# Kernel optimization log

Hardware: AMD Instinct MI355X
Metric: run time of the kernel (lower is better)

Reference implementation:

```python
import jax, jax.numpy as jnp
import numpy as np

NUM_HEADS = 8
HIDDEN = 128
MAX_NEIGHBORS = 64
BATCH = 8192


def setup_inputs() -> dict:
    key = jax.random.key(0)
    ks = jax.random.split(key, 4)
    query = jax.random.normal(ks[0], (BATCH, MAX_NEIGHBORS, HIDDEN), dtype=jnp.float32)
    value = jax.random.normal(ks[1], (BATCH, 1, HIDDEN), dtype=jnp.float32)
    # per-head Dense(hidden) weights (glorot-ish scale) + zero biases
    Wa = jax.random.normal(ks[2], (NUM_HEADS, HIDDEN, HIDDEN), dtype=jnp.float32) * (1.0 / np.sqrt(HIDDEN))
    ba = jnp.zeros((NUM_HEADS, HIDDEN), dtype=jnp.float32)
    Wo = jax.random.normal(ks[3], (NUM_HEADS * HIDDEN, HIDDEN), dtype=jnp.float32) * (1.0 / np.sqrt(NUM_HEADS * HIDDEN))
    bo = jnp.zeros((HIDDEN,), dtype=jnp.float32)
    return {"query": query, "value": value, "Wa": Wa, "ba": ba, "Wo": Wo, "bo": bo}


def reference(query, value, Wa, ba, Wo, bo):
    # query: [B, N, H], value: [B, 1, H]
    q = jnp.concatenate([query, value], axis=1)  # [B, N+1, H]
    contexts = []
    for i in range(NUM_HEADS):
        # sequential per-head projection of the running query tensor
        q = jnp.einsum('bnh,hk->bnk', q, Wa[i]) + ba[i]          # [B, N+1, H]
        e = jnp.einsum('boh,bnh->bon', value, q)                 # [B, 1, N+1]
        scores = jax.nn.softmax(e, axis=-1)                      # [B, 1, N+1]
        contexts.append(jnp.einsum('bon,bnh->boh', scores, q))   # [B, 1, H]
    ctx = jnp.concatenate(contexts, axis=-1)                     # [B, 1, num_heads*H]
    x = jnp.einsum('boc,ck->bok', ctx, Wo) + bo                  # [B, 1, H]
    return jax.nn.relu(x)
```

## Files before the change

kernel.cpp:

```cpp
#include <hip/hip_runtime.h>
#include <math.h>

#define WS_P  0
#define WS_Q0 65536
#define WS_Q1 81920
#define WS_R  98304
#define WS_WT 114688
#define WS_WU 245760
#define WS_ZT 376832
#define WS_Z0 507904
#define WS_U  524288
#define WS_PO 8912896

struct MMJob { const float* A; const float* B; float* C; float* wu; };
struct MMArgs { MMJob j[8]; };

__device__ __forceinline__ float dpp_xor1(float x) {
  return __int_as_float(__builtin_amdgcn_update_dpp(0, __float_as_int(x), 0xB1, 0xF, 0xF, false));
}
__device__ __forceinline__ float dpp_xor2(float x) {
  return __int_as_float(__builtin_amdgcn_update_dpp(0, __float_as_int(x), 0x4E, 0xF, 0xF, false));
}
__device__ __forceinline__ float dpp_xor8(float x) {
  return __int_as_float(__builtin_amdgcn_update_dpp(0, __float_as_int(x), 0x128, 0xF, 0xF, false));
}
__device__ __forceinline__ float readlane_f(float v, int n) {
  return __int_as_float(__builtin_amdgcn_readlane(__float_as_int(v), n));
}

__device__ void mm128_job(const MMJob J, const int tile, const int t, float* Al) {
  const int col = t & 127;
  const int rg = t >> 7;
  if (J.A == nullptr) {
    for (int rr = 0; rr < 16; ++rr) {
      const int r = tile * 32 + rg * 16 + rr;
      const float v = J.B[r * 128 + col];
      if (J.C) J.C[r * 128 + col] = v;
      if (J.wu) J.wu[col * 1024 + r] = v;
    }
    return;
  }
  for (int jj = 0; jj < 16; ++jj) {
    const int idx = t + jj * 256;
    Al[idx] = J.A[tile * 32 * 128 + idx];
  }
  __syncthreads();
  float acc[16];
#pragma unroll
  for (int rr = 0; rr < 16; ++rr) acc[rr] = 0.f;
  for (int h = 0; h < 128; ++h) {
    const float bv = J.B[h * 128 + col];
#pragma unroll
    for (int rr = 0; rr < 16; ++rr)
      acc[rr] = fmaf(Al[(rg * 16 + rr) * 128 + h], bv, acc[rr]);
  }
#pragma unroll
  for (int rr = 0; rr < 16; ++rr) {
    const int r = tile * 32 + rg * 16 + rr;
    if (J.C) J.C[r * 128 + col] = acc[rr];
    if (J.wu) J.wu[col * 1024 + r] = acc[rr];
  }
}

__global__ __launch_bounds__(256) void mm128_jobs(MMArgs args) {
  __shared__ float smem[4096];
  mm128_job(args.j[blockIdx.x >> 2], blockIdx.x & 3, threadIdx.x, smem);
}

__device__ void bias_z0_dev(const float* __restrict__ Wa, const float* __restrict__ ba,
                            const float* __restrict__ Wo, const float* __restrict__ bo,
                            float* __restrict__ z0, const int t, float* smem) {
  float* bt = smem;
  float* zpart = smem + 1024;
  if (t < 128) bt[t] = ba[t];
  __syncthreads();
  for (int i = 1; i < 8; ++i) {
    if (t < 128) {
      float v = ba[i * 128 + t];
      for (int h = 0; h < 128; ++h)
        v = fmaf(bt[(i - 1) * 128 + h], Wa[i * 16384 + h * 128 + t], v);
      bt[i * 128 + t] = v;
    }
    __syncthreads();
  }
  const int col = t & 127, half = t >> 7;
  float z = half ? 0.f : bo[col];
  for (int i = half * 4; i < half * 4 + 4; ++i)
    for (int h = 0; h < 128; ++h)
      z = fmaf(bt[i * 128 + h], Wo[(i * 128 + h) * 128 + col], z);
  zpart[half * 128 + col] = z;
  __syncthreads();
  if (t < 128) z0[t] = zpart[t] + zpart[128 + t];
}

__device__ void gemm_U_dev(const float* __restrict__ V, const float* __restrict__ WU,
                           float* __restrict__ U, const int bid, const int t, float* Vl) {
  const int rt = bid >> 3;
  const int ct = bid & 7;
  const int cg = t & 7;
  const int rg = t >> 3;
  const int r0 = rt * 128;
  float4 acc[4][4];
#pragma unroll
  for (int a = 0; a < 4; ++a)
#pragma unroll
    for (int c = 0; c < 4; ++c) acc[a][c] = make_float4(0.f, 0.f, 0.f, 0.f);
  for (int kc = 0; kc < 4; ++kc) {
    __syncthreads();
    {
      const int srow = t >> 3, k8 = t & 7;
#pragma unroll
      for (int pp = 0; pp < 4; ++pp) {
        const int rr = pp * 32 + srow;
        *(float4*)&Vl[rr * 33 + k8 * 4] =
            *(const float4*)&V[(size_t)(r0 + rr) * 128 + kc * 32 + k8 * 4];
      }
    }
    __syncthreads();
#pragma unroll 4
    for (int kk = 0; kk < 32; ++kk) {
      const float* wrow = WU + (size_t)(kc * 32 + kk) * 1024 + ct * 128 + cg * 16;
      const float4 w0 = *(const float4*)(wrow + 0);
      const float4 w1 = *(const float4*)(wrow + 4);
      const float4 w2 = *(const float4*)(wrow + 8);
      const float4 w3 = *(const float4*)(wrow + 12);
#pragma unroll
      for (int r = 0; r < 4; ++r) {
        const float s = Vl[(rg * 4 + r) * 33 + kk];
        acc[r][0].x = fmaf(s, w0.x, acc[r][0].x); acc[r][0].y = fmaf(s, w0.y, acc[r][0].y);
        acc[r][0].z = fmaf(s, w0.z, acc[r][0].z); acc[r][0].w = fmaf(s, w0.w, acc[r][0].w);
        acc[r][1].x = fmaf(s, w1.x, acc[r][1].x); acc[r][1].y = fmaf(s, w1.y, acc[r][1].y);
        acc[r][1].z = fmaf(s, w1.z, acc[r][1].z); acc[r][1].w = fmaf(s, w1.w, acc[r][1].w);
        acc[r][2].x = fmaf(s, w2.x, acc[r][2].x); acc[r][2].y = fmaf(s, w2.y, acc[r][2].y);
        acc[r][2].z = fmaf(s, w2.z, acc[r][2].z); acc[r][2].w = fmaf(s, w2.w, acc[r][2].w);
        acc[r][3].x = fmaf(s, w3.x, acc[r][3].x); acc[r][3].y = fmaf(s, w3.y, acc[r][3].y);
        acc[r][3].z = fmaf(s, w3.z, acc[r][3].z); acc[r][3].w = fmaf(s, w3.w, acc[r][3].w);
      }
    }
  }
#pragma unroll
  for (int r = 0; r < 4; ++r) {
    float* urow = U + (size_t)(r0 + rg * 4 + r) * 1024 + ct * 128 + cg * 16;
    *(float4*)(urow + 0) = acc[r][0];
    *(float4*)(urow + 4) = acc[r][1];
    *(float4*)(urow + 8) = acc[r][2];
    *(float4*)(urow + 12) = acc[r][3];
  }
}

__global__ __launch_bounds__(256) void k4_combo(MMArgs args,
    const float* __restrict__ V, const float* __restrict__ WU, float* __restrict__ U,
    const float* __restrict__ Wa, const float* __restrict__ ba,
    const float* __restrict__ Wo, const float* __restrict__ bo,
    float* __restrict__ z0) {
  __shared__ float smem[4224];
  const int bid = blockIdx.x;
  if (bid < 32) mm128_job(args.j[bid >> 2], bid & 3, threadIdx.x, smem);
  else if (bid < 544) gemm_U_dev(V, WU, U, bid - 32, threadIdx.x, smem);
  else bias_z0_dev(Wa, ba, Wo, bo, z0, threadIdx.x, smem);
}

__global__ __launch_bounds__(256, 4) void attn_main_k(
    const float* __restrict__ query, const float* __restrict__ value,
    float* __restrict__ U) {
  __shared__ float epart[8 * 66];
  __shared__ float spart[4 * 1024];
  const int b = blockIdx.x;
  const int t = threadIdx.x;
  const int w = t >> 6;
  const int l = t & 63;

  const int sel1 = l & 1, sel2 = (l >> 1) & 1, sel8 = (l >> 3) & 1;
  const int g = ((l >> 2) & 1) | (((l >> 4) & 1) << 1) | (((l >> 5) & 1) << 2);
  const int myhead = 4 * sel1 + 2 * sel2 + sel8;

  float2 u2[8];
  {
    const float* ub = U + (size_t)b * 1024 + 2 * l;
#pragma unroll
    for (int jj = 0; jj < 8; ++jj) u2[jj] = *(const float2*)(ub + ((myhead ^ jj) << 7));
  }
  float2 q2[16];
  {
    const float* qb = query + (size_t)b * 8192 + (size_t)(w * 16) * 128 + 2 * l;
#pragma unroll
    for (int r = 0; r < 16; ++r) q2[r] = *(const float2*)(qb + r * 128);
  }
  const float2 v2 = *(const float2*)(value + (size_t)b * 128 + 2 * l);

  auto epass = [&](const float2 qv, const int n) {
    float p[8];
#pragma unroll
    for (int i = 0; i < 8; ++i) p[i] = fmaf(qv.y, u2[i].y, qv.x * u2[i].x);
    float a4[4];
#pragma unroll
    for (int i = 0; i < 4; ++i) a4[i] = p[i] + dpp_xor1(p[i + 4]);
    float a2v[2];
#pragma unroll
    for (int i = 0; i < 2; ++i) a2v[i] = a4[i] + dpp_xor2(a4[i + 2]);
    float e = a2v[0] + dpp_xor8(a2v[1]);
    e += __shfl_xor(e, 4);
    e += __shfl_xor(e, 16);
    e += __shfl_xor(e, 32);
    if (g == 0) epart[myhead * 66 + n] = e;
  };
#pragma unroll
  for (int r = 0; r < 16; ++r) epass(q2[r], 16 * w + r);
  if (w == 0) epass(v2, 64);
  __syncthreads();

  float sc[8], c64[8];
  {
#pragma unroll
    for (int i = 0; i < 8; ++i) {
      const float x = epart[i * 66 + l];
      const float x64 = epart[i * 66 + 64];
      float m = x;
      m = fmaxf(m, dpp_xor1(m));
      m = fmaxf(m, dpp_xor2(m));
      m = fmaxf(m, __shfl_xor(m, 4));
      m = fmaxf(m, dpp_xor8(m));
      m = fmaxf(m, __shfl_xor(m, 16));
      m = fmaxf(m, __shfl_xor(m, 32));
      m = fmaxf(m, x64);
      const float p = __expf(x - m);
      const float p64 = __expf(x64 - m);
      float ss = p;
      ss += dpp_xor1(ss);
      ss += dpp_xor2(ss);
      ss += __shfl_xor(ss, 4);
      ss += dpp_xor8(ss);
      ss += __shfl_xor(ss, 16);
      ss += __shfl_xor(ss, 32);
      ss += p64;
      const float inv = 1.0f / ss;
      sc[i] = p * inv;
      c64[i] = p64 * inv;
    }
  }

  float2 s2[8];
#pragma unroll
  for (int i = 0; i < 8; ++i) s2[i] = make_float2(0.f, 0.f);
#pragma unroll
  for (int r = 0; r < 16; ++r) {
    const int n = 16 * w + r;
#pragma unroll
    for (int i = 0; i < 8; ++i) {
      const float cwv = readlane_f(sc[i], n);
      s2[i].x = fmaf(cwv, q2[r].x, s2[i].x);
      s2[i].y = fmaf(cwv, q2[r].y, s2[i].y);
    }
  }
  if (w == 0) {
#pragma unroll
    for (int i = 0; i < 8; ++i) {
      s2[i].x = fmaf(c64[i], v2.x, s2[i].x);
      s2[i].y = fmaf(c64[i], v2.y, s2[i].y);
    }
  }
#pragma unroll
  for (int i = 0; i < 8; ++i)
    *(float2*)&spart[w * 1024 + i * 128 + 2 * l] = s2[i];
  __syncthreads();
  float4 acc = make_float4(0.f, 0.f, 0.f, 0.f);
#pragma unroll
  for (int w4 = 0; w4 < 4; ++w4) {
    const float4 pp = *(const float4*)&spart[w4 * 1024 + t * 4];
    acc.x += pp.x; acc.y += pp.y; acc.z += pp.z; acc.w += pp.w;
  }
  *(float4*)(U + (size_t)b * 1024 + t * 4) = acc;
}

__global__ __launch_bounds__(256) void gemm_out_k(
    const float* __restrict__ S, const float* __restrict__ Z,
    float* __restrict__ P0, float* __restrict__ PW) {
  __shared__ float STl[64 * 68];
  const int rb = blockIdx.x >> 2;
  const int kc = blockIdx.x & 3;
  const int t = threadIdx.x;
  const int rg = t >> 4;
  const int cg = t & 15;
  float4 acc[4][2];
#pragma unroll
  for (int r = 0; r < 4; ++r) {
    acc[r][0] = make_float4(0.f, 0.f, 0.f, 0.f);
    acc[r][1] = make_float4(0.f, 0.f, 0.f, 0.f);
  }
  for (int sub = 0; sub < 4; ++sub) {
    const int kb = kc * 256 + sub * 64;
    __syncthreads();
#pragma unroll
    for (int j = 0; j < 4; ++j) {
      const int i4 = t + j * 256;
      const int row = i4 >> 4, kq = i4 & 15;
      const float4 s4 = *(const float4*)&S[(size_t)(rb * 64 + row) * 1024 + kb + kq * 4];
      STl[(kq * 4 + 0) * 68 + row] = s4.x;
      STl[(kq * 4 + 1) * 68 + row] = s4.y;
      STl[(kq * 4 + 2) * 68 + row] = s4.z;
      STl[(kq * 4 + 3) * 68 + row] = s4.w;
    }
    __syncthreads();
#pragma unroll 4
    for (int k = 0; k < 64; ++k) {
      const float4 sa = *(const float4*)&STl[k * 68 + rg * 4];
      const float* zr = Z + (size_t)(kb + k) * 128 + cg * 8;
      const float4 za = *(const float4*)zr;
      const float4 zb = *(const float4*)(zr + 4);
      const float sr[4] = {sa.x, sa.y, sa.z, sa.w};
#pragma unroll
      for (int r = 0; r < 4; ++r) {
        acc[r][0].x = fmaf(sr[r], za.x, acc[r][0].x);
        acc[r][0].y = fmaf(sr[r], za.y, acc[r][0].y);
        acc[r][0].z = fmaf(sr[r], za.z, acc[r][0].z);
        acc[r][0].w = fmaf(sr[r], za.w, acc[r][0].w);
        acc[r][1].x = fmaf(sr[r], zb.x, acc[r][1].x);
        acc[r][1].y = fmaf(sr[r], zb.y, acc[r][1].y);
        acc[r][1].z = fmaf(sr[r], zb.z, acc[r][1].z);
        acc[r][1].w = fmaf(sr[r], zb.w, acc[r][1].w);
      }
    }
  }
  float* P = (kc == 0) ? P0 : (PW + (size_t)(kc - 1) * 1048576);
#pragma unroll
  for (int r = 0; r < 4; ++r) {
    float* prow = P + (size_t)(rb * 64 + rg * 4 + r) * 128 + cg * 8;
    *(float4*)(prow + 0) = acc[r][0];
    *(float4*)(prow + 4) = acc[r][1];
  }
}

__global__ __launch_bounds__(256) void reduce_relu_k(
    float* __restrict__ out, const float* __restrict__ PW,
    const float* __restrict__ z0) {
  const int idx = blockIdx.x * 256 + threadIdx.x;
  const float4 z4 = *(const float4*)&z0[(idx & 31) * 4];
  float4 a = ((const float4*)out)[idx];
  const float4 p1 = ((const float4*)(PW + 0 * 1048576))[idx];
  const float4 p2 = ((const float4*)(PW + 1 * 1048576))[idx];
  const float4 p3 = ((const float4*)(PW + 2 * 1048576))[idx];
  a.x = fmaxf(a.x + p1.x + p2.x + p3.x + z4.x, 0.f);
  a.y = fmaxf(a.y + p1.y + p2.y + p3.y + z4.y, 0.f);
  a.z = fmaxf(a.z + p1.z + p2.z + p3.z + z4.z, 0.f);
  a.w = fmaxf(a.w + p1.w + p2.w + p3.w + z4.w, 0.f);
  ((float4*)out)[idx] = a;
}

extern "C" void kernel_launch(void* const* d_in, const int* in_sizes, int n_in,
                              void* d_out, int out_size, void* d_ws, size_t ws_size,
                              hipStream_t stream) {
  const float* query = (const float*)d_in[0];
  const float* value = (const float*)d_in[1];
  const float* Wa    = (const float*)d_in[2];
  const float* ba    = (const float*)d_in[3];
  const float* Wo    = (const float*)d_in[4];
  const float* bo    = (const float*)d_in[5];
  float* ws = (float*)d_ws;
  float* P  = ws + WS_P;
  float* Q0 = ws + WS_Q0;
  float* Q1 = ws + WS_Q1;
  float* R  = ws + WS_R;
  float* WT = ws + WS_WT;
  float* WU = ws + WS_WU;
  float* ZT = ws + WS_ZT;
  float* Z0 = ws + WS_Z0;
  float* U  = ws + WS_U;
  float* PW = ws + WS_PO;

  MMArgs a1{};
  for (int j = 0; j < 4; ++j)
    a1.j[j] = MMJob{Wa + 2 * j * 16384, Wa + (2 * j + 1) * 16384, P + j * 16384, nullptr};
  mm128_jobs<<<16, 256, 0, stream>>>(a1);

  MMArgs a2{};
  a2.j[0] = MMJob{P, P + 16384, Q0, nullptr};
  a2.j[1] = MMJob{P + 2 * 16384, P + 3 * 16384, Q1, nullptr};
  a2.j[2] = MMJob{P + 2 * 16384, Wa + 6 * 16384, R, nullptr};
  mm128_jobs<<<12, 256, 0, stream>>>(a2);

  MMArgs a3{};
  a3.j[0] = MMJob{nullptr, Wa,             WT + 0 * 16384, WU + 0 * 128};
  a3.j[1] = MMJob{nullptr, P,              WT + 1 * 16384, WU + 1 * 128};
  a3.j[2] = MMJob{P,       Wa + 2 * 16384, WT + 2 * 16384, WU + 2 * 128};
  a3.j[3] = MMJob{nullptr, Q0,             WT + 3 * 16384, WU + 3 * 128};
  a3.j[4] = MMJob{Q0,      Wa + 4 * 16384, WT + 4 * 16384, WU + 4 * 128};
  a3.j[5] = MMJob{Q0,      P + 2 * 16384,  WT + 5 * 16384, WU + 5 * 128};
  a3.j[6] = MMJob{Q0,      R,              WT + 6 * 16384, WU + 6 * 128};
  a3.j[7] = MMJob{Q0,      Q1,             WT + 7 * 16384, WU + 7 * 128};
  mm128_jobs<<<32, 256, 0, stream>>>(a3);

  MMArgs a4{};
  for (int i = 0; i < 8; ++i)
    a4.j[i] = MMJob{WT + i * 16384, Wo + i * 16384, ZT + i * 16384, nullptr};
  k4_combo<<<545, 256, 0, stream>>>(a4, value, WU, U, Wa, ba, Wo, bo, Z0);

  attn_main_k<<<8192, 256, 0, stream>>>(query, value, U);

  gemm_out_k<<<512, 256, 0, stream>>>(U, ZT, (float*)d_out, PW);
  reduce_relu_k<<<1024, 256, 0, stream>>>((float*)d_out, PW, Z0);
}
```

Baseline: 234.7 us.

## Assign one batch row per wavefront in attention kernel, removing block syncs

Restructures the attention kernel so each 64-lane wave processes a full batch row, streaming query in 16-row chunks instead of splitting rows across four waves. This removes the __syncthreads barriers and the shared-memory cross-wave partial-sum reduction, and cuts the grid to 2048 blocks. In exchange, the query row is loaded twice from global memory (once for scores, once for the weighted sum). This risks doubling HBM traffic on a memory-bound kernel if the re-read misses cache.

Result: slower. 261.2 us (+11.3%).

```diff
diff --git a/kernel.cpp b/kernel.cpp
--- a/kernel.cpp
+++ b/kernel.cpp
@@ -160,15 +160,15 @@
   else bias_z0_dev(Wa, ba, Wo, bo, z0, threadIdx.x, smem);
 }
 
-__global__ __launch_bounds__(256, 4) void attn_main_k(
+__global__ __launch_bounds__(256, 4) void attn_wave_k(
     const float* __restrict__ query, const float* __restrict__ value,
     float* __restrict__ U) {
-  __shared__ float epart[8 * 66];
-  __shared__ float spart[4 * 1024];
-  const int b = blockIdx.x;
+  __shared__ float etab[4 * 544];
   const int t = threadIdx.x;
   const int w = t >> 6;
   const int l = t & 63;
+  const int b = blockIdx.x * 4 + w;
+  float* et = etab + w * 544;
 
   const int sel1 = l & 1, sel2 = (l >> 1) & 1, sel8 = (l >> 3) & 1;
   const int g = ((l >> 2) & 1) | (((l >> 4) & 1) << 1) | (((l >> 5) & 1) << 2);
@@ -180,12 +180,7 @@
 #pragma unroll
     for (int jj = 0; jj < 8; ++jj) u2[jj] = *(const float2*)(ub + ((myhead ^ jj) << 7));
   }
-  float2 q2[16];
-  {
-    const float* qb = query + (size_t)b * 8192 + (size_t)(w * 16) * 128 + 2 * l;
-#pragma unroll
-    for (int r = 0; r < 16; ++r) q2[r] = *(const float2*)(qb + r * 128);
-  }
+  const float* qb = query + (size_t)b * 8192 + 2 * l;
   const float2 v2 = *(const float2*)(value + (size_t)b * 128 + 2 * l);
 
   auto epass = [&](const float2 qv, const int n) {
@@ -202,74 +197,77 @@
     e += __shfl_xor(e, 4);
     e += __shfl_xor(e, 16);
     e += __shfl_xor(e, 32);
-    if (g == 0) epart[myhead * 66 + n] = e;
+    if (g == 0) et[myhead * 66 + n] = e;
   };
-#pragma unroll
-  for (int r = 0; r < 16; ++r) epass(q2[r], 16 * w + r);
-  if (w == 0) epass(v2, 64);
-  __syncthreads();
+
+#pragma unroll 1
+  for (int c = 0; c < 4; ++c) {
+    float2 qc[16];
+#pragma unroll
+    for (int r = 0; r < 16; ++r) qc[r] = *(const float2*)(qb + (c * 16 + r) * 128);
+#pragma unroll
+    for (int r = 0; r < 16; ++r) epass(qc[r], c * 16 + r);
+  }
+  epass(v2, 64);
+  asm volatile("s_waitcnt lgkmcnt(0)" ::: "memory");
 
   float sc[8], c64[8];
+#pragma unroll
+  for (int i = 0; i < 8; ++i) {
+    const float x = et[i * 66 + l];
+    const float x64 = et[i * 66 + 64];
+    float m = x;
+    m = fmaxf(m, dpp_xor1(m));
+    m = fmaxf(m, dpp_xor2(m));
+    m = fmaxf(m, __shfl_xor(m, 4));
+    m = fmaxf(m, dpp_xor8(m));
+    m = fmaxf(m, __shfl_xor(m, 16));
+    m = fmaxf(m, __shfl_xor(m, 32));
+    m = fmaxf(m, x64);
+    const float p = __expf(x - m);
+    const float p64 = __expf(x64 - m);
+    float ss = p;
+    ss += dpp_xor1(ss);
+    ss += dpp_xor2(ss);
+    ss += __shfl_xor(ss, 4);
+    ss += dpp_xor8(ss);
+    ss += __shfl_xor(ss, 16);
+    ss += __shfl_xor(ss, 32);
+    ss += p64;
+    const float inv = 1.0f / ss;
+    sc[i] = p * inv;
+    c64[i] = p64 * inv;
+  }
+
+  float2 s2[8];
+#pragma unroll
+  for (int i = 0; i < 8; ++i) s2[i] = make_float2(0.f, 0.f);
+#pragma unroll 1
+  for (int c = 0; c < 4; ++c) {
+    float2 qc[16];
+#pragma unroll
+    for (int r = 0; r < 16; ++r) qc[r] = *(const float2*)(qb + (c * 16 + r) * 128);
+#pragma unroll
+    for (int r = 0; r < 16; ++r) {
+      const int n = c * 16 + r;
+#pragma unroll
+      for (int i = 0; i < 8; ++i) {
+        const float cwv = readlane_f(sc[i], n);
+        s2[i].x = fmaf(cwv, qc[r].x, s2[i].x);
+        s2[i].y = fmaf(cwv, qc[r].y, s2[i].y);
+      }
+    }
+  }
+#pragma unroll
+  for (int i = 0; i < 8; ++i) {
+    s2[i].x = fmaf(c64[i], v2.x, s2[i].x);
+    s2[i].y = fmaf(c64[i], v2.y, s2[i].y);
+  }
   {
-#pragma unroll
-    for (int i = 0; i < 8; ++i) {
-      const float x = epart[i * 66 + l];
-      const float x64 = epart[i * 66 + 64];
-      float m = x;
-      m = fmaxf(m, dpp_xor1(m));
-      m = fmaxf(m, dpp_xor2(m));
-      m = fmaxf(m, __shfl_xor(m, 4));
-      m = fmaxf(m, dpp_xor8(m));
-      m = fmaxf(m, __shfl_xor(m, 16));
-      m = fmaxf(m, __shfl_xor(m, 32));
-      m = fmaxf(m, x64);
-      const float p = __expf(x - m);
-      const float p64 = __expf(x64 - m);
-      float ss = p;
-      ss += dpp_xor1(ss);
-      ss += dpp_xor2(ss);
-      ss += __shfl_xor(ss, 4);
-      ss += dpp_xor8(ss);
-      ss += __shfl_xor(ss, 16);
-      ss += __shfl_xor(ss, 32);
-      ss += p64;
-      const float inv = 1.0f / ss;
-      sc[i] = p * inv;
-      c64[i] = p64 * inv;
-    }
-  }
-
-  float2 s2[8];
-#pragma unroll
-  for (int i = 0; i < 8; ++i) s2[i] = make_float2(0.f, 0.f);
-#pragma unroll
-  for (int r = 0; r < 16; ++r) {
-    const int n = 16 * w + r;
-#pragma unroll
-    for (int i = 0; i < 8; ++i) {
-      const float cwv = readlane_f(sc[i], n);
-      s2[i].x = fmaf(cwv, q2[r].x, s2[i].x);
-      s2[i].y = fmaf(cwv, q2[r].y, s2[i].y);
-    }
-  }
-  if (w == 0) {
-#pragma unroll
-    for (int i = 0; i < 8; ++i) {
-      s2[i].x = fmaf(c64[i], v2.x, s2[i].x);
-      s2[i].y = fmaf(c64[i], v2.y, s2[i].y);
-    }
-  }
-#pragma unroll
-  for (int i = 0; i < 8; ++i)
-    *(float2*)&spart[w * 1024 + i * 128 + 2 * l] = s2[i];
-  __syncthreads();
-  float4 acc = make_float4(0.f, 0.f, 0.f, 0.f);
-#pragma unroll
-  for (int w4 = 0; w4 < 4; ++w4) {
-    const float4 pp = *(const float4*)&spart[w4 * 1024 + t * 4];
-    acc.x += pp.x; acc.y += pp.y; acc.z += pp.z; acc.w += pp.w;
-  }
-  *(float4*)(U + (size_t)b * 1024 + t * 4) = acc;
+    float* ob = U + (size_t)b * 1024 + 2 * l;
+#pragma unroll
+    for (int i = 0; i < 8; ++i) *(float2*)(ob + i * 128) = s2[i];
+  }
 }
 
 __global__ __launch_bounds__(256) void gemm_out_k(
@@ -394,7 +392,7 @@
     a4.j[i] = MMJob{WT + i * 16384, Wo + i * 16384, ZT + i * 16384, nullptr};
   k4_combo<<<545, 256, 0, stream>>>(a4, value, WU, U, Wa, ba, Wo, bo, Z0);
 
-  attn_main_k<<<8192, 256, 0, stream>>>(query, value, U);
+  attn_wave_k<<<2048, 256, 0, stream>>>(query, value, U);
 
   gemm_out_k<<<512, 256, 0, stream>>>(U, ZT, (float*)d_out, PW);
   reduce_relu_k<<<1024, 256, 0, stream>>>((float*)d_out, PW, Z0);
```
